# Performance work log

Hardware: AMD Instinct MI355X
Metric: run time of the kernel (lower is better)

The kernel has to match this reference:

```python
import jax, jax.numpy as jnp
import numpy as np

B, L, D, H = 8, 2048, 1024, 1024
BASE_LR, BASE_WD = 0.01, 0.9


def setup_inputs() -> dict:
    key = jax.random.key(0)
    ks = jax.random.split(key, 8)
    s = 1.0 / np.sqrt(D)
    return {
        "x": jax.random.normal(ks[0], (B, L, D), jnp.float32),
        "hidden": jax.random.normal(ks[1], (B, D, H), jnp.float32),
        "log_base_lr": jnp.array([np.log(BASE_LR)], jnp.float32),
        "w_lr": jax.random.normal(ks[2], (D, 1), jnp.float32) * s,
        "b_lr": jnp.zeros((1,), jnp.float32),
        "log_base_wd": jnp.array([np.log(BASE_WD)], jnp.float32),
        "w_wd": jax.random.normal(ks[3], (D, 1), jnp.float32) * s,
        "b_wd": jnp.zeros((1,), jnp.float32),
        "w_q": jax.random.normal(ks[4], (D, H), jnp.float32) * s,
        "b_q": jnp.zeros((H,), jnp.float32),
        "w_k": jax.random.normal(ks[5], (D, H), jnp.float32) * s,
        "b_k": jnp.zeros((H,), jnp.float32),
        "w_v": jax.random.normal(ks[6], (D, D), jnp.float32) * s,
        "b_v": jnp.zeros((D,), jnp.float32),
    }


def reference(x, hidden, log_base_lr, w_lr, b_lr, log_base_wd, w_wd, b_wd,
              w_q, b_q, w_k, b_k, w_v, b_v):
    batch, length, dim = x.shape
    W_prev = hidden  # [b, d, h]
    query = x @ w_q + b_q                     # [b, l, h]
    key = x @ w_k + b_k                       # [b, l, h]
    value = x @ w_v + b_v                     # [b, l, d]
    lr = jnp.exp(log_base_lr) * jax.nn.sigmoid((x @ w_lr + b_lr)[..., 0])  # [b, l]
    # log(1 - base_wd * sigmoid(.)) via log1p for stability; same math.
    log_wd = jnp.log1p(-jnp.exp(log_base_wd) * jax.nn.sigmoid((x @ w_wd + b_wd)[..., 0]))  # [b, l]
    wd_cross = jnp.exp(jnp.cumsum(log_wd, axis=1))  # [b, l]
    # inner-chunk decay: entry [b, m, l] = exp(sum_{j=m+1..l} log_wd[b, j]) for l >= m
    tri = jnp.triu(jnp.broadcast_to(log_wd[:, None, :], (batch, length, length)), k=1)
    wd_inner = jnp.triu(jnp.exp(jnp.cumsum(tri, axis=2)))  # [b, l, l]
    kq = jnp.einsum('bld,bmd->blm', key, query)            # [b, l, m]
    mask_kq = kq * wd_inner
    WpK_V = jnp.einsum('bdh,blh->bld', W_prev, key) - value  # [b, l, d]
    y_inner = -jnp.einsum('bld,bl,blm->bmd', WpK_V, lr, mask_kq)
    y_cross = jnp.einsum('bdh,blh,bl->bld', W_prev, query, wd_cross)
    y = y_inner + y_cross
    W_next_inner = -jnp.einsum('bld,bl,blh->bdh', WpK_V, lr * wd_inner[:, :, -1], key)
    W_next_cross = W_prev * wd_cross[:, -1][:, None, None]
    W_next = W_next_inner + W_next_cross
    return y, W_next
```

## Files before the change

kernel.cpp:

```cpp
#include <hip/hip_runtime.h>
#include <stdint.h>

#define BB 8
#define LL 2048
#define DD 1024
#define HH 1024
#define BL (BB*LL)

typedef __attribute__((ext_vector_type(8))) short short8;
typedef __attribute__((ext_vector_type(4))) float f32x4;

__device__ __forceinline__ unsigned short f2bf(float f) {
  unsigned int x = __float_as_uint(f);
  unsigned int r = (x + 0x7fffu + ((x >> 16) & 1u)) >> 16;
  return (unsigned short)r;
}
__device__ __forceinline__ float bf2f(unsigned short u) {
  return __uint_as_float(((unsigned int)u) << 16);
}

__device__ __forceinline__ void stage16(const unsigned short* g, unsigned short* l) {
  __builtin_amdgcn_global_load_lds((const __attribute__((address_space(1))) void*)g,
                                   (__attribute__((address_space(3))) void*)l,
                                   16, 0, 0);
}

struct __align__(16) Smem8 {
  unsigned short a[2][16384];
  unsigned short b[2][16384];
};
static_assert(sizeof(Smem8) == 131072, "LDS size");

__device__ __forceinline__ void acc_init8(f32x4 (&acc)[8][4]) {
#pragma unroll
  for (int i = 0; i < 8; ++i)
#pragma unroll
    for (int j = 0; j < 4; ++j)
      acc[i][j] = (f32x4){0.f, 0.f, 0.f, 0.f};
}

template<class FA, class FB>
__device__ __forceinline__ void gemm8_core(FA srcA, FB srcB, int NK,
                                           Smem8* sm, f32x4 (&acc)[8][4]) {
  const int lane = threadIdx.x & 63;
  const int wave = threadIdx.x >> 6;
  const int srow = lane >> 3;
  const int scol = ((lane & 7) ^ srow) * 8;
  const int fk = (lane >> 4) * 8;
  const int fr = lane & 15;
  const int fx = fr & 7;
  const int mwr = (wave >> 2) * 128;
  const int nwr = (wave & 3) * 64;
  const int cA0 = (wave < 4) ? 2 * wave : 2 * wave + 8;
  const int cA1 = cA0 + 8;
  const int cB0 = (wave >> 1) * 8 + 2 * (wave & 1);
  const int cB1 = cB0 + 4;

  auto SA = [&](int p, int kt, int c) {
    stage16(srcA(c * 8 + srow, kt) + scol, &sm->a[p][c * 512]);
    stage16(srcA(c * 8 + 8 + srow, kt) + scol, &sm->a[p][(c + 1) * 512]);
  };
  auto SB = [&](int p, int kt, int c) {
    stage16(srcB(c * 8 + srow, kt) + scol, &sm->b[p][c * 512]);
    stage16(srcB(c * 8 + 8 + srow, kt) + scol, &sm->b[p][(c + 1) * 512]);
  };
  short8 af[4][2], bfv[2][2];
  auto LDA = [&](int p, int ih) {
#pragma unroll
    for (int i = 0; i < 4; ++i)
#pragma unroll
      for (int kk = 0; kk < 2; ++kk) {
        const int kc = ((((kk * 32 + fk) >> 3) ^ fx) << 3);
        af[i][kk] = *(const short8*)&sm->a[p][(mwr + ih * 64 + i * 16 + fr) * 64 + kc];
      }
  };
  auto LDB = [&](int p, int jh) {
#pragma unroll
    for (int j = 0; j < 2; ++j)
#pragma unroll
      for (int kk = 0; kk < 2; ++kk) {
        const int kc = ((((kk * 32 + fk) >> 3) ^ fx) << 3);
        bfv[j][kk] = *(const short8*)&sm->b[p][(nwr + jh * 32 + j * 16 + fr) * 64 + kc];
      }
  };
  auto MM = [&](int ih, int jh) {
#pragma unroll
    for (int i = 0; i < 4; ++i)
#pragma unroll
      for (int j = 0; j < 2; ++j)
#pragma unroll
        for (int kk = 0; kk < 2; ++kk)
          acc[ih * 4 + i][jh * 2 + j] = __builtin_amdgcn_mfma_f32_16x16x32_bf16(
              af[i][kk], bfv[j][kk], acc[ih * 4 + i][jh * 2 + j], 0, 0, 0);
  };

#define PH(IH, JH, ...) do { \
    __VA_ARGS__ \
    __builtin_amdgcn_sched_barrier(0); \
    __builtin_amdgcn_s_barrier(); \
    asm volatile("s_waitcnt lgkmcnt(0)" ::: "memory"); \
    __builtin_amdgcn_sched_barrier(0); \
    __builtin_amdgcn_s_setprio(1); \
    MM(IH, JH); \
    __builtin_amdgcn_s_setprio(0); \
    __builtin_amdgcn_sched_barrier(0); \
    __builtin_amdgcn_s_barrier(); \
    __builtin_amdgcn_sched_barrier(0); \
  } while (0)

  if (NK > 1) {
    SA(0, 0, cA0); SA(0, 0, cA1); SB(0, 0, cB0); SB(0, 0, cB1);
    SB(1, 1, cB0); SA(1, 1, cA0);
    asm volatile("s_waitcnt vmcnt(4)" ::: "memory");
  } else {
    SA(0, 0, cA0); SA(0, 0, cA1); SB(0, 0, cB0); SB(0, 0, cB1);
    asm volatile("s_waitcnt vmcnt(0)" ::: "memory");
  }
  __builtin_amdgcn_sched_barrier(0);
  __builtin_amdgcn_s_barrier();
  __builtin_amdgcn_sched_barrier(0);

  for (int t = 0; t < NK; ++t) {
    const int p = t & 1, po = p ^ 1;
    const bool s1 = (t + 1 < NK), s2 = (t + 2 < NK);
    PH(0, 0, LDA(p, 0); LDB(p, 0); if (s1) SA(po, t + 1, cA1); );
    PH(1, 0, LDA(p, 1);            if (s1) SB(po, t + 1, cB1); );
    PH(0, 1, LDA(p, 0); LDB(p, 1); if (s2) SB(p, t + 2, cB0); );
    PH(1, 1, LDA(p, 1);
             if (s2) SA(p, t + 2, cA0);
             if (s2)      { asm volatile("s_waitcnt vmcnt(4)" ::: "memory"); }
             else if (s1) { asm volatile("s_waitcnt vmcnt(0)" ::: "memory"); } );
  }
#undef PH
}

template<typename F>
__device__ __forceinline__ void epi8(const f32x4 (&acc)[8][4], F body) {
  const int lane = threadIdx.x & 63;
  const int wave = threadIdx.x >> 6;
  const int mwr = (wave >> 2) * 128, nwr = (wave & 3) * 64;
#pragma unroll
  for (int i = 0; i < 8; ++i)
#pragma unroll
    for (int j = 0; j < 4; ++j)
#pragma unroll
      for (int jj = 0; jj < 4; ++jj)
        body(mwr + i * 16 + ((lane >> 4) << 2) + jj,
             nwr + j * 16 + (lane & 15), acc[i][j][jj]);
}


__global__ void k_prep_x(const float* __restrict__ x, const float* __restrict__ wlr,
                         const float* __restrict__ wwd, unsigned short* __restrict__ xb,
                         float* __restrict__ lrlog, float* __restrict__ wdlog) {
  const int wave = threadIdx.x >> 6, lane = threadIdx.x & 63;
  const int row = blockIdx.x * 4 + wave;
  const float* xr = x + (size_t)row * DD;
  float s1 = 0.f, s2 = 0.f;
#pragma unroll
  for (int ch = 0; ch < 4; ++ch) {
    const int col = ch * 256 + lane * 4;
    float4 v = *(const float4*)(xr + col);
    float4 a = *(const float4*)(wlr + col);
    float4 b = *(const float4*)(wwd + col);
    s1 += v.x*a.x + v.y*a.y + v.z*a.z + v.w*a.w;
    s2 += v.x*b.x + v.y*b.y + v.z*b.z + v.w*b.w;
    uint2 u;
    u.x = (unsigned)f2bf(v.x) | ((unsigned)f2bf(v.y) << 16);
    u.y = (unsigned)f2bf(v.z) | ((unsigned)f2bf(v.w) << 16);
    *(uint2*)(xb + (size_t)row * DD + col) = u;
  }
#pragma unroll
  for (int off = 32; off > 0; off >>= 1) {
    s1 += __shfl_down(s1, off);
    s2 += __shfl_down(s2, off);
  }
  if (lane == 0) { lrlog[row] = s1; wdlog[row] = s2; }
}

__global__ void k_prep_w(const float* __restrict__ wq, const float* __restrict__ wk,
                         const float* __restrict__ wv, unsigned short* __restrict__ wqt,
                         unsigned short* __restrict__ wkt, unsigned short* __restrict__ wvtn,
                         unsigned short* __restrict__ wkr) {
  const int idx = blockIdx.x * 256 + threadIdx.x;
  if (blockIdx.z == 3) { wkr[idx] = f2bf(wk[idx]); return; }
  const int k = idx >> 10, n = idx & 1023;
  const float* src = (blockIdx.z == 0) ? wq : (blockIdx.z == 1) ? wk : wv;
  unsigned short* dst = (blockIdx.z == 0) ? wqt : (blockIdx.z == 1) ? wkt : wvtn;
  float v = src[(size_t)k * 1024 + n];
  if (blockIdx.z == 2) v = -v;
  dst[(size_t)n * 1024 + k] = f2bf(v);
}

__global__ void k_prep_h(const float* __restrict__ hid, unsigned short* __restrict__ wpb) {
  const size_t i = ((size_t)blockIdx.x * 256 + threadIdx.x) * 4;
  float4 v = *(const float4*)(hid + i);
  uint2 u;
  u.x = (unsigned)f2bf(v.x) | ((unsigned)f2bf(v.y) << 16);
  u.y = (unsigned)f2bf(v.z) | ((unsigned)f2bf(v.w) << 16);
  *(uint2*)(wpb + i) = u;
}

__global__ void k_bias2(const unsigned short* __restrict__ wpb, const float* __restrict__ bk,
                        const float* __restrict__ bv, float* __restrict__ bias2) {
  const int wave = threadIdx.x >> 6, lane = threadIdx.x & 63;
  const int row = blockIdx.x * 4 + wave;
  const unsigned short* wr = wpb + (size_t)row * HH;
  float s = 0.f;
#pragma unroll
  for (int ch = 0; ch < 4; ++ch) {
    const int col = ch * 256 + lane * 4;
    float4 a = *(const float4*)(bk + col);
    ushort4 u = *(const ushort4*)(wr + col);
    s += a.x * bf2f(u.x) + a.y * bf2f(u.y) + a.z * bf2f(u.z) + a.w * bf2f(u.w);
  }
#pragma unroll
  for (int off = 32; off > 0; off >>= 1) s += __shfl_down(s, off);
  if (lane == 0) bias2[row] = s - bv[row & 1023];
}

__global__ void k_scan(const float* __restrict__ lrlog, const float* __restrict__ wdlog,
                       const float* __restrict__ lbl, const float* __restrict__ blr,
                       const float* __restrict__ lbw, const float* __restrict__ bwd,
                       float* __restrict__ lr, float* __restrict__ c,
                       float* __restrict__ s, float* __restrict__ ecl) {
  const int b = blockIdx.x, t = threadIdx.x;
  __shared__ float sums[256];
  const float elr = expf(lbl[0]);
  const float ewd = expf(lbw[0]);
  const float blr0 = blr[0], bwd0 = bwd[0];
  float lw[8];
  const float* wb = wdlog + (size_t)b * LL + t * 8;
  float tot = 0.f;
#pragma unroll
  for (int i = 0; i < 8; ++i) {
    float z = wb[i] + bwd0;
    float sig = 1.f / (1.f + expf(-z));
    tot += log1pf(-ewd * sig);
    lw[i] = tot;
  }
  sums[t] = tot;
  __syncthreads();
  for (int off = 1; off < 256; off <<= 1) {
    float v = (t >= off) ? sums[t - off] : 0.f;
    __syncthreads();
    sums[t] += v;
    __syncthreads();
  }
  const float prev = (t > 0) ? sums[t - 1] : 0.f;
  const float ctot = sums[255];
  const float* lb = lrlog + (size_t)b * LL + t * 8;
#pragma unroll
  for (int i = 0; i < 8; ++i) {
    const int idx = b * LL + t * 8 + i;
    const float ci = prev + lw[i];
    c[idx] = ci;
    float zl = lb[i] + blr0;
    float lri = elr / (1.f + expf(-zl));
    lr[idx] = lri;
    s[idx] = lri * expf(ctot - ci);
  }
  if (t == 0) ecl[b] = expf(ctot);
}


__global__ __launch_bounds__(512, 2) void k8_gemm_m2(const unsigned short* __restrict__ wpb,
    const unsigned short* __restrict__ wkr, const unsigned short* __restrict__ wvtn,
    unsigned short* __restrict__ w2t) {
  __shared__ Smem8 sm;
  const int b = blockIdx.x;
  const int mt = blockIdx.y & 3, nt = blockIdx.y >> 2;
  const int m0 = mt * 256, n0 = nt * 256;
  f32x4 acc[8][4]; acc_init8(acc);
  gemm8_core(
    [&](int r, int kt) { return wpb + (size_t)b * DD * HH + (size_t)(m0 + r) * HH + kt * 64; },
    [&](int r, int kt) { return wkr + (size_t)(n0 + r) * HH + kt * 64; },
    HH / 64, &sm, acc);
  epi8(acc, [&](int rr, int cc, float av) {
    const size_t gi = (size_t)(m0 + rr) * DD + (n0 + cc);
    w2t[(size_t)b * DD * DD + gi] = f2bf(av + bf2f(wvtn[gi]));
  });
}

__global__ __launch_bounds__(512, 2) void k8_gemm_q(const unsigned short* __restrict__ xb,
    const unsigned short* __restrict__ wt, const float* __restrict__ bias,
    const float* __restrict__ c, unsigned short* __restrict__ outb,
    unsigned short* __restrict__ q2b) {
  __shared__ Smem8 sm;
  const int mt = blockIdx.x * 8 + (blockIdx.y & 7);
  const int nt = blockIdx.y >> 3;
  const int m0 = mt * 256, n0 = nt * 256;
  f32x4 acc[8][4]; acc_init8(acc);
  gemm8_core(
    [&](int r, int kt) { return xb + (size_t)(m0 + r) * DD + kt * 64; },
    [&](int r, int kt) { return wt + (size_t)(n0 + r) * DD + kt * 64; },
    DD / 64, &sm, acc);
  const int lane = threadIdx.x & 63, wave = threadIdx.x >> 6;
  const int mwr = (wave >> 2) * 128, nwr = (wave & 3) * 64;
  float er[8][4];
#pragma unroll
  for (int i = 0; i < 8; ++i)
#pragma unroll
    for (int jj = 0; jj < 4; ++jj)
      er[i][jj] = __expf(c[m0 + mwr + i * 16 + ((lane >> 4) << 2) + jj]);
#pragma unroll
  for (int i = 0; i < 8; ++i)
#pragma unroll
    for (int j = 0; j < 4; ++j)
#pragma unroll
      for (int jj = 0; jj < 4; ++jj) {
        const int row = m0 + mwr + i * 16 + ((lane >> 4) << 2) + jj;
        const int col = n0 + nwr + j * 16 + (lane & 15);
        const float v = acc[i][j][jj] + bias[col];
        outb[(size_t)row * HH + col] = f2bf(v);
        q2b[(size_t)row * HH + col] = f2bf(v * er[i][jj]);
      }
}

__global__ __launch_bounds__(512, 2) void k8_gemm_k(const unsigned short* __restrict__ xb,
    const unsigned short* __restrict__ wt, const float* __restrict__ bias,
    const float* __restrict__ s, unsigned short* __restrict__ kb,
    unsigned short* __restrict__ k2t) {
  __shared__ Smem8 sm;
  const int mt = blockIdx.x * 8 + (blockIdx.y & 7);
  const int nt = blockIdx.y >> 3;
  const int m0 = mt * 256, n0 = nt * 256;
  f32x4 acc[8][4]; acc_init8(acc);
  gemm8_core(
    [&](int r, int kt) { return xb + (size_t)(m0 + r) * DD + kt * 64; },
    [&](int r, int kt) { return wt + (size_t)(n0 + r) * DD + kt * 64; },
    DD / 64, &sm, acc);
  const int lane = threadIdx.x & 63, wave = threadIdx.x >> 6;
  const int mwr = (wave >> 2) * 128, nwr = (wave & 3) * 64;
#pragma unroll
  for (int i = 0; i < 8; ++i)
#pragma unroll
    for (int j = 0; j < 4; ++j) {
      const int col = n0 + nwr + j * 16 + (lane & 15);
      const float bias_c = bias[col];
      const int row0 = m0 + mwr + i * 16 + ((lane >> 4) << 2);
      const int b = row0 >> 11, ml0 = row0 & 2047;
      unsigned short tmp[4];
#pragma unroll
      for (int jj = 0; jj < 4; ++jj) {
        float v = acc[i][j][jj] + bias_c;
        kb[(size_t)(row0 + jj) * HH + col] = f2bf(v);
        tmp[jj] = f2bf(v * s[row0 + jj]);
      }
      uint2 u;
      u.x = (unsigned)tmp[0] | ((unsigned)tmp[1] << 16);
      u.y = (unsigned)tmp[2] | ((unsigned)tmp[3] << 16);
      *(uint2*)&k2t[((size_t)b * HH + col) * LL + ml0] = u;
    }
}

__global__ __launch_bounds__(512, 2) void k8_gemm_u(const unsigned short* __restrict__ xb,
    const unsigned short* __restrict__ w2t, const float* __restrict__ bias2,
    unsigned short* __restrict__ ut) {
  __shared__ Smem8 sm;
  const int b = blockIdx.x;
  const int mt = blockIdx.x * 8 + (blockIdx.y & 7);
  const int nt = blockIdx.y >> 3;
  const int m0 = mt * 256, n0 = nt * 256;
  f32x4 acc[8][4]; acc_init8(acc);
  gemm8_core(
    [&](int r, int kt) { return xb + (size_t)(m0 + r) * DD + kt * 64; },
    [&](int r, int kt) { return w2t + (size_t)b * DD * DD + (size_t)(n0 + r) * DD + kt * 64; },
    DD / 64, &sm, acc);
  const int lane = threadIdx.x & 63, wave = threadIdx.x >> 6;
  const int mwr = (wave >> 2) * 128, nwr = (wave & 3) * 64;
#pragma unroll
  for (int i = 0; i < 8; ++i)
#pragma unroll
    for (int j = 0; j < 4; ++j) {
      const int col = n0 + nwr + j * 16 + (lane & 15);
      const float b2c = bias2[b * DD + col];
      const int row0 = m0 + mwr + i * 16 + ((lane >> 4) << 2);
      const int ml0 = row0 & 2047;
      unsigned short tmp[4];
#pragma unroll
      for (int jj = 0; jj < 4; ++jj) tmp[jj] = f2bf(acc[i][j][jj] + b2c);
      uint2 u;
      u.x = (unsigned)tmp[0] | ((unsigned)tmp[1] << 16);
      u.y = (unsigned)tmp[2] | ((unsigned)tmp[3] << 16);
      *(uint2*)&ut[((size_t)b * DD + col) * LL + ml0] = u;
    }
}

__global__ __launch_bounds__(512, 2) void k8_gemm_p(const unsigned short* __restrict__ qb,
    const unsigned short* __restrict__ kb, const float* __restrict__ lr,
    const float* __restrict__ c, unsigned short* __restrict__ pb) {
  __shared__ Smem8 sm;
  const int b = blockIdx.x;
  const int t = blockIdx.y;
  int mt = (int)((sqrtf(8.f * (float)t + 1.f) - 1.f) * 0.5f);
  while ((mt + 1) * (mt + 2) / 2 <= t) ++mt;
  while (mt * (mt + 1) / 2 > t) --mt;
  const int nt = t - mt * (mt + 1) / 2;
  const int base = b * LL;
  const int m0 = mt * 256, n0 = nt * 256;
  f32x4 acc[8][4]; acc_init8(acc);
  gemm8_core(
    [&](int rr, int kt) { return qb + (size_t)(base + m0 + rr) * HH + kt * 64; },
    [&](int rr, int kt) { return kb + (size_t)(base + n0 + rr) * HH + kt * 64; },
    HH / 64, &sm, acc);
  const int lane = threadIdx.x & 63, wave = threadIdx.x >> 6;
  const int mwr = (wave >> 2) * 128, nwr = (wave & 3) * 64;
  if (nt != mt) {
    const float cref = c[base + m0];
    float er[8][4], fc[4];
#pragma unroll
    for (int i = 0; i < 8; ++i)
#pragma unroll
      for (int jj = 0; jj < 4; ++jj)
        er[i][jj] = __expf(c[base + m0 + mwr + i * 16 + ((lane >> 4) << 2) + jj] - cref);
#pragma unroll
    for (int j = 0; j < 4; ++j) {
      const int l = n0 + nwr + j * 16 + (lane & 15);
      fc[j] = lr[base + l] * __expf(cref - c[base + l]);
    }
#pragma unroll
    for (int i = 0; i < 8; ++i)
#pragma unroll
      for (int j = 0; j < 4; ++j) {
        const int l = n0 + nwr + j * 16 + (lane & 15);
        const int row0 = m0 + mwr + i * 16 + ((lane >> 4) << 2);
#pragma unroll
        for (int jj = 0; jj < 4; ++jj) {
          const float v = -acc[i][j][jj] * er[i][jj] * fc[j];
          pb[((size_t)base + row0 + jj) * LL + l] = f2bf(v);
        }
      }
  } else {
    epi8(acc, [&](int rr, int cc, float av) {
      const int m = m0 + rr, l = n0 + cc;
      float v = 0.f;
      if (l <= m) v = -av * lr[base + l] * __expf(c[base + m] - c[base + l]);
      pb[((size_t)base + m) * LL + l] = f2bf(v);
    });
  }
}

__global__ __launch_bounds__(512, 2) void k8_gemm_y(const unsigned short* __restrict__ pb,
    const unsigned short* __restrict__ ut, const unsigned short* __restrict__ q2b,
    const unsigned short* __restrict__ wpb, float* __restrict__ out) {
  __shared__ Smem8 sm;
  const int b = blockIdx.x;
  const int mt = blockIdx.y & 7;
  const int nt = blockIdx.y >> 3;
  const int m0 = mt * 256, n0 = nt * 256;
  const int NK1 = (mt + 1) * 4;
  f32x4 acc[8][4]; acc_init8(acc);
  gemm8_core(
    [&](int r, int kt) {
      return (kt < NK1) ? pb + (size_t)b * LL * LL + (size_t)(m0 + r) * LL + kt * 64
                        : q2b + ((size_t)b * LL + m0 + r) * HH + (kt - NK1) * 64;
    },
    [&](int r, int kt) {
      return (kt < NK1) ? ut + (size_t)b * DD * LL + (size_t)(n0 + r) * LL + kt * 64
                        : wpb + (size_t)b * DD * HH + (size_t)(n0 + r) * HH + (kt - NK1) * 64;
    },
    NK1 + 16, &sm, acc);
  epi8(acc, [&](int rr, int cc, float av) {
    out[((size_t)b * LL + m0 + rr) * DD + (n0 + cc)] = av;
  });
}

__global__ __launch_bounds__(512, 2) void k8_gemm_wn(const unsigned short* __restrict__ ut,
    const unsigned short* __restrict__ k2t, const float* __restrict__ hid,
    const float* __restrict__ ecl, float* __restrict__ out2) {
  __shared__ Smem8 sm;
  const int b = blockIdx.x;
  const int mt = blockIdx.y & 3, nt = blockIdx.y >> 2;
  const int m0 = mt * 256, n0 = nt * 256;
  f32x4 acc[8][4]; acc_init8(acc);
  gemm8_core(
    [&](int r, int kt) { return ut + (size_t)b * DD * LL + (size_t)(m0 + r) * LL + kt * 64; },
    [&](int r, int kt) { return k2t + (size_t)b * HH * LL + (size_t)(n0 + r) * LL + kt * 64; },
    LL / 64, &sm, acc);
  const float eclb = ecl[b];
  epi8(acc, [&](int rr, int cc, float av) {
    const size_t gi = ((size_t)b * DD + (m0 + rr)) * HH + (n0 + cc);
    out2[gi] = -av + eclb * hid[gi];
  });
}


extern "C" void kernel_launch(void* const* d_in, const int* in_sizes, int n_in,
                              void* d_out, int out_size, void* d_ws, size_t ws_size,
                              hipStream_t stream) {
  (void)in_sizes; (void)n_in; (void)out_size; (void)ws_size;
  const float* x   = (const float*)d_in[0];
  const float* hid = (const float*)d_in[1];
  const float* lbl = (const float*)d_in[2];
  const float* wlr = (const float*)d_in[3];
  const float* blr = (const float*)d_in[4];
  const float* lbw = (const float*)d_in[5];
  const float* wwd = (const float*)d_in[6];
  const float* bwd = (const float*)d_in[7];
  const float* wq  = (const float*)d_in[8];
  const float* bq  = (const float*)d_in[9];
  const float* wk  = (const float*)d_in[10];
  const float* bk  = (const float*)d_in[11];
  const float* wv  = (const float*)d_in[12];
  const float* bv  = (const float*)d_in[13];
  float* out = (float*)d_out;

  char* w = (char*)d_ws;
  constexpr size_t SZ_XB  = (size_t)BL * DD * 2;
  constexpr size_t SZ_QB  = (size_t)BL * HH * 2;
  constexpr size_t SZ_KB  = (size_t)BL * HH * 2;
  constexpr size_t SZ_K2T = (size_t)BB * HH * LL * 2;
  constexpr size_t SZ_UT  = (size_t)BB * DD * LL * 2;
  constexpr size_t SZ_PB  = (size_t)BB * LL * LL * 2;
  constexpr size_t SZ_WT  = (size_t)DD * HH * 2;
  constexpr size_t SZ_WPB = (size_t)BB * DD * HH * 2;
  constexpr size_t SZ_V16 = (size_t)BL * 4;

  size_t off = 0;
  unsigned short* xb   = (unsigned short*)(w + off); off += SZ_XB;
  unsigned short* qb   = (unsigned short*)(w + off); off += SZ_QB;
  unsigned short* kb   = (unsigned short*)(w + off); off += SZ_KB;
  unsigned short* k2t  = (unsigned short*)(w + off); off += SZ_K2T;
  unsigned short* ut   = (unsigned short*)(w + off); off += SZ_UT;
  unsigned short* pb   = (unsigned short*)(w + off); off += SZ_PB;
  unsigned short* wqt  = (unsigned short*)(w + off); off += SZ_WT;
  unsigned short* wkt  = (unsigned short*)(w + off); off += SZ_WT;
  unsigned short* wvtn = (unsigned short*)(w + off); off += SZ_WT;
  unsigned short* wpb  = (unsigned short*)(w + off); off += SZ_WPB;
  float* lrlog = (float*)(w + off); off += SZ_V16;
  float* wdlog = (float*)(w + off); off += SZ_V16;
  float* lr    = (float*)(w + off); off += SZ_V16;
  float* c     = (float*)(w + off); off += SZ_V16;
  float* s     = (float*)(w + off); off += SZ_V16;
  float* ecl   = (float*)(w + off); off += 256;
  float* bias2 = (float*)(w + off); off += (size_t)BB * DD * 4;

  unsigned short* w2t = pb;
  unsigned short* wkr = pb + (size_t)BB * DD * DD;

  unsigned short* q2b = (unsigned short*)(out + (size_t)BL * DD);
  float* out2 = out + (size_t)BL * DD;

  k_prep_x<<<dim3(BL / 4), 256, 0, stream>>>(x, wlr, wwd, xb, lrlog, wdlog);
  k_prep_w<<<dim3(4096, 1, 4), 256, 0, stream>>>(wq, wk, wv, wqt, wkt, wvtn, wkr);
  k_prep_h<<<dim3((unsigned)((size_t)BB * DD * HH / 1024)), 256, 0, stream>>>(hid, wpb);
  k_scan<<<dim3(BB), 256, 0, stream>>>(lrlog, wdlog, lbl, blr, lbw, bwd, lr, c, s, ecl);
  k_bias2<<<dim3(BB * DD / 4), 256, 0, stream>>>(wpb, bk, bv, bias2);

  k8_gemm_m2<<<dim3(8, 16), 512, 0, stream>>>(wpb, wkr, wvtn, w2t);
  k8_gemm_q<<<dim3(8, 32), 512, 0, stream>>>(xb, wqt, bq, c, qb, q2b);
  k8_gemm_k<<<dim3(8, 32), 512, 0, stream>>>(xb, wkt, bk, s, kb, k2t);
  k8_gemm_u<<<dim3(8, 32), 512, 0, stream>>>(xb, w2t, bias2, ut);
  k8_gemm_p<<<dim3(8, 36), 512, 0, stream>>>(qb, kb, lr, c, pb);
  k8_gemm_y<<<dim3(8, 32), 512, 0, stream>>>(pb, ut, q2b, wpb, out);
  k8_gemm_wn<<<dim3(8, 16), 512, 0, stream>>>(ut, k2t, hid, ecl, out2);
}
```

Baseline: 649.4 us.

## Restructure GEMM main loop into k-split phases with fewer barriers

The bf16 MFMA GEMM main loop drops the four-phase schedule, which had two workgroup barriers per phase. It now loads all B fragments once per k-tile and walks A in k-halves, with two barriers per tile instead of eight. The prefetch order changes: both A chunks of the next tile are staged up front, and both B chunks two tiles ahead are staged mid-tile. Fewer barriers and larger MFMA batches should cut sync stalls, at the cost of more registers held for B fragments and a new LDS buffer-reuse ordering that must still be race-free.

```diff
diff --git a/kernel.cpp b/kernel.cpp
--- a/kernel.cpp
+++ b/kernel.cpp
@@ -64,56 +64,39 @@
     stage16(srcB(c * 8 + srow, kt) + scol, &sm->b[p][c * 512]);
     stage16(srcB(c * 8 + 8 + srow, kt) + scol, &sm->b[p][(c + 1) * 512]);
   };
-  short8 af[4][2], bfv[2][2];
-  auto LDA = [&](int p, int ih) {
+  const int kc0 = (((fk >> 3) ^ fx) << 3);
+  const int kc1 = ((((32 + fk) >> 3) ^ fx) << 3);
+
+  short8 af[4], bfv[4][2];
+  auto LDB = [&](int p) {
+#pragma unroll
+    for (int j = 0; j < 4; ++j) {
+      bfv[j][0] = *(const short8*)&sm->b[p][(nwr + j * 16 + fr) * 64 + kc0];
+      bfv[j][1] = *(const short8*)&sm->b[p][(nwr + j * 16 + fr) * 64 + kc1];
+    }
+  };
+  auto LDA4 = [&](int p, int ih, int kc) {
 #pragma unroll
     for (int i = 0; i < 4; ++i)
-#pragma unroll
-      for (int kk = 0; kk < 2; ++kk) {
-        const int kc = ((((kk * 32 + fk) >> 3) ^ fx) << 3);
-        af[i][kk] = *(const short8*)&sm->a[p][(mwr + ih * 64 + i * 16 + fr) * 64 + kc];
-      }
+      af[i] = *(const short8*)&sm->a[p][(mwr + ih * 64 + i * 16 + fr) * 64 + kc];
   };
-  auto LDB = [&](int p, int jh) {
-#pragma unroll
-    for (int j = 0; j < 2; ++j)
-#pragma unroll
-      for (int kk = 0; kk < 2; ++kk) {
-        const int kc = ((((kk * 32 + fk) >> 3) ^ fx) << 3);
-        bfv[j][kk] = *(const short8*)&sm->b[p][(nwr + jh * 32 + j * 16 + fr) * 64 + kc];
-      }
+  auto MMk = [&](int ih, int kk) {
+#pragma unroll
+    for (int i = 0; i < 4; ++i)
+#pragma unroll
+      for (int j = 0; j < 4; ++j)
+        acc[ih * 4 + i][j] = __builtin_amdgcn_mfma_f32_16x16x32_bf16(
+            af[i], bfv[j][kk], acc[ih * 4 + i][j], 0, 0, 0);
   };
-  auto MM = [&](int ih, int jh) {
-#pragma unroll
-    for (int i = 0; i < 4; ++i)
-#pragma unroll
-      for (int j = 0; j < 2; ++j)
-#pragma unroll
-        for (int kk = 0; kk < 2; ++kk)
-          acc[ih * 4 + i][jh * 2 + j] = __builtin_amdgcn_mfma_f32_16x16x32_bf16(
-              af[i][kk], bfv[j][kk], acc[ih * 4 + i][jh * 2 + j], 0, 0, 0);
-  };
-
-#define PH(IH, JH, ...) do { \
-    __VA_ARGS__ \
-    __builtin_amdgcn_sched_barrier(0); \
-    __builtin_amdgcn_s_barrier(); \
-    asm volatile("s_waitcnt lgkmcnt(0)" ::: "memory"); \
-    __builtin_amdgcn_sched_barrier(0); \
-    __builtin_amdgcn_s_setprio(1); \
-    MM(IH, JH); \
-    __builtin_amdgcn_s_setprio(0); \
-    __builtin_amdgcn_sched_barrier(0); \
-    __builtin_amdgcn_s_barrier(); \
-    __builtin_amdgcn_sched_barrier(0); \
-  } while (0)
-
+
+#define LGKM0 do { asm volatile("s_waitcnt lgkmcnt(0)" ::: "memory"); \
+                   __builtin_amdgcn_sched_barrier(0); } while (0)
+
+  SA(0, 0, cA0); SA(0, 0, cA1); SB(0, 0, cB0); SB(0, 0, cB1);
   if (NK > 1) {
-    SA(0, 0, cA0); SA(0, 0, cA1); SB(0, 0, cB0); SB(0, 0, cB1);
-    SB(1, 1, cB0); SA(1, 1, cA0);
+    SB(1, 1, cB0); SB(1, 1, cB1);
     asm volatile("s_waitcnt vmcnt(4)" ::: "memory");
   } else {
-    SA(0, 0, cA0); SA(0, 0, cA1); SB(0, 0, cB0); SB(0, 0, cB1);
     asm volatile("s_waitcnt vmcnt(0)" ::: "memory");
   }
   __builtin_amdgcn_sched_barrier(0);
@@ -123,15 +106,32 @@
   for (int t = 0; t < NK; ++t) {
     const int p = t & 1, po = p ^ 1;
     const bool s1 = (t + 1 < NK), s2 = (t + 2 < NK);
-    PH(0, 0, LDA(p, 0); LDB(p, 0); if (s1) SA(po, t + 1, cA1); );
-    PH(1, 0, LDA(p, 1);            if (s1) SB(po, t + 1, cB1); );
-    PH(0, 1, LDA(p, 0); LDB(p, 1); if (s2) SB(p, t + 2, cB0); );
-    PH(1, 1, LDA(p, 1);
-             if (s2) SA(p, t + 2, cA0);
-             if (s2)      { asm volatile("s_waitcnt vmcnt(4)" ::: "memory"); }
-             else if (s1) { asm volatile("s_waitcnt vmcnt(0)" ::: "memory"); } );
-  }
-#undef PH
+    if (s1) { SA(po, t + 1, cA0); SA(po, t + 1, cA1); }
+    LDB(p);
+    LDA4(p, 0, kc0);
+    LGKM0;
+    __builtin_amdgcn_s_setprio(1); MMk(0, 0); __builtin_amdgcn_s_setprio(0);
+    LDA4(p, 0, kc1);
+    LGKM0;
+    __builtin_amdgcn_s_setprio(1); MMk(0, 1); __builtin_amdgcn_s_setprio(0);
+    __builtin_amdgcn_sched_barrier(0);
+    __builtin_amdgcn_s_barrier();
+    __builtin_amdgcn_sched_barrier(0);
+    if (s2) { SB(p, t + 2, cB0); SB(p, t + 2, cB1); }
+    LDA4(p, 1, kc0);
+    LGKM0;
+    __builtin_amdgcn_s_setprio(1); MMk(1, 0); __builtin_amdgcn_s_setprio(0);
+    LDA4(p, 1, kc1);
+    LGKM0;
+    __builtin_amdgcn_s_setprio(1); MMk(1, 1); __builtin_amdgcn_s_setprio(0);
+    __builtin_amdgcn_sched_barrier(0);
+    if (s2)      { asm volatile("s_waitcnt vmcnt(4)" ::: "memory"); }
+    else if (s1) { asm volatile("s_waitcnt vmcnt(0)" ::: "memory"); }
+    __builtin_amdgcn_sched_barrier(0);
+    __builtin_amdgcn_s_barrier();
+    __builtin_amdgcn_sched_barrier(0);
+  }
+#undef LGKM0
 }
 
 template<typename F>
```

After: 610.1 us. 1.06x faster.
